# Performance work log

Measured on AMD Instinct MI355X. Metric: run time of the kernel, lower is better.

## Reference

```python
import math
import jax, jax.numpy as jnp
import numpy as np

# --- static config (matches init_kwargs) ---
BS, NIND, NSTEP, NDIM, ORDER, NEQ, NIVS, NIV = 128, 8, 64, 1, 2, 1, 2, 2
B = BS * NIND          # batch_size
K = ORDER + 1          # n_orders
S = NSTEP              # n_steps
T = S - 1
D = NDIM * K           # vars per step block
N = S * D              # total variables (without eps column)
NVARS = N + 1          # +1 eps column at index 0


def _smooth_indices():
    """Static (row, col) COO indices of the smoothness-constraint matrix,
    in the exact order the torch module emits values (forward, central, backward)."""
    def rav(st, dim, o):
        return (st * NDIM + dim) * K + o + 1  # +1 for eps column
    rows, cols, r = [], [], 0
    for st in range(T):                      # forward Taylor constraints
        for dim in range(NDIM):
            for i in range(K - 1):
                rows += [r, r]; cols += [0, rav(st + 1, dim, i)]
                for j in range(i, K):
                    rows.append(r); cols.append(rav(st, dim, j))
                r += 1
    for st in range(1, S - 1):               # central difference constraints
        for dim in range(NDIM):
            rows += [r] * 4
            cols += [0, rav(st - 1, dim, K - 2), rav(st + 1, dim, K - 2), rav(st, dim, K - 1)]
            r += 1
    for st in range(T):                      # backward Taylor constraints
        for dim in range(NDIM):
            for i in range(K - 1):
                rows += [r, r]; cols += [0, rav(st, dim, i)]
                for j in range(i, K):
                    rows.append(r); cols.append(rav(st + 1, dim, j))
                r += 1
    return np.asarray(rows), np.asarray(cols), r

ROWS, COLS, NROWS = _smooth_indices()
INIT_IDX = (np.arange(NDIM)[:, None] * K + np.arange(NIV)[None, :]).reshape(-1)
BLK = np.arange(S)[:, None] * D + np.arange(D)[None, :]  # (S, D) block row/col ids


def _derivative_A(steps):
    """Dense derivative-constraint matrix A: (B, NROWS, N) (eps column dropped)."""
    s = steps                                 # (B, T)
    ones = jnp.ones_like(s)
    fw, bw = [], []
    for i in range(K - 1):
        ss = -(s ** i)
        fw += [ones, ss]
        bw += [ones, ss if i % 2 == 0 else -ss]
        for j in range(i, K):
            v = s ** j / math.factorial(j - i)
            fw.append(v)
            bw.append(v if j % 2 == 0 else -v)
    fv = jnp.stack(fw, axis=-1).reshape(s.shape[0], -1)   # (B, T*L)
    bv = jnp.stack(bw, axis=-1).reshape(s.shape[0], -1)
    cp = s[:, 1:] + s[:, :-1]                             # csteps + psteps, (B, T-1)
    cv = jnp.stack([jnp.ones_like(cp), -cp ** (K - 3), cp ** (K - 3), -cp ** (K - 2)],
                   axis=-1).reshape(s.shape[0], -1)
    vals = jnp.concatenate([fv, cv, bv], axis=-1)          # (B, nnz)
    A_full = jnp.zeros((s.shape[0], NROWS, NVARS), dtype=s.dtype).at[:, ROWS, COLS].add(vals)
    return A_full[:, :, 1:]


def setup_inputs() -> dict:
    key = jax.random.key(0)
    k1, k2, k3, k4 = jax.random.split(key, 4)
    coeffs = jax.random.normal(k1, (B, S, NEQ, NDIM, K), dtype=jnp.float32)
    rhs = jax.random.normal(k2, (B, S, NEQ), dtype=jnp.float32)
    iv_rhs = jax.random.normal(k3, (B, NIVS, NDIM, NIV), dtype=jnp.float32)
    steps = jax.random.uniform(k4, (B, T), dtype=jnp.float32, minval=0.1, maxval=1.0)
    return {"coeffs": coeffs, "rhs": rhs, "iv_rhs": iv_rhs, "steps": steps}


def reference(coeffs, rhs, iv_rhs, steps):
    A = _derivative_A(steps)                                # (B, NROWS, N)
    Ae = coeffs.reshape(B, S, NEQ, D)
    AetAe = jnp.einsum('bsei,bsej->bsij', Ae, Ae)           # (B, S, D, D)
    Aetbe = jnp.einsum('bsei,bse->bsi', Ae, rhs)            # (B, S, D)
    # initial-value regularization on first NIVS step blocks
    AetAe = AetAe.at[:, :NIVS, INIT_IDX, INIT_IDX].add(1.0)
    bi = jnp.pad(iv_rhs, ((0, 0), (0, 0), (0, 0), (0, K - NIV))).reshape(B, NIVS, D)
    Aetbe = Aetbe.at[:, :NIVS, :].add(bi)
    # block-diagonal embedding of AetAe into the full NxN system
    dense = jnp.zeros((B, N, N), dtype=coeffs.dtype).at[:, BLK[:, :, None], BLK[:, None, :]].set(AetAe)
    AtA = jnp.einsum('bri,brj->bij', A, A) + dense          # (B, N, N) SPD
    Lc = jnp.linalg.cholesky(AtA)
    x = jax.scipy.linalg.cho_solve((Lc, True), Aetbe.reshape(B, N, 1))[..., 0]
    return x.reshape(B, S, NDIM, K)
```

## Files before the change

kernel.cpp:

```cpp
#include <hip/hip_runtime.h>
#include <math.h>

#define NB 1024
#define NS 64
#define NT 63
#define NV 192
#define BW 7
#define NC 314

#define NW 32
#define BP_PER_W (31*16)
#define L_PER_W  (93*8)
#define XQ_PER_W 96

__global__ __launch_bounds__(1024, 1)
void ode_mega(const float* __restrict__ coeffs,
              const float* __restrict__ rhs,
              const float* __restrict__ steps,
              const float* __restrict__ iv_rhs,
              float* __restrict__ wsBP,
              float* __restrict__ wsL,
              float* __restrict__ wsXq,
              float* __restrict__ out)
{
    const int w   = blockIdx.x;
    const int tid = threadIdx.x;

    __shared__ float cf[32 * 193];
    __shared__ float sl[32 * 65];
    __shared__ float rl[32 * 65];
    __shared__ float il[128];
    __shared__ float midl[27 * 32];
    __shared__ float mxl[6 * 32];

    for (int idx = tid; idx < 32 * 192; idx += 1024) {
        const int b = idx / 192, j = idx - 192 * b;
        cf[b * 193 + j] = coeffs[(size_t)w * 6144 + idx];
    }
    for (int idx = tid; idx < 32 * 63; idx += 1024) {
        const int b = idx / 63, j = idx - 63 * b;
        sl[b * 65 + j] = steps[(size_t)w * 2016 + idx];
    }
    for (int idx = tid; idx < 32 * 64; idx += 1024) {
        const int b = idx >> 6, j = idx & 63;
        rl[b * 65 + j] = rhs[(size_t)w * 2048 + idx];
    }
    if (tid < 128) il[tid] = iv_rhs[(size_t)w * 128 + tid];
    __syncthreads();

    for (int idx = tid; idx < 31 * 32; idx += 1024) {
        const int it = idx >> 5;
        const int pr = idx & 31;
        const float* cfp = cf + pr * 193;
        const float* slp = sl + pr * 65;
        const float* rlp = rl + pr * 65;

        float F[16], G[16];
        {
            const int t = it;
            const float c0 = cfp[3*t], c1 = cfp[3*t+1], c2 = cfp[3*t+2];
            const float r  = rlp[t];
            const float p  = (t >= 1) ? slp[t-1] : 0.f;
            const float s  = slp[t];
            const float sn = slp[t+1];
            const float mP = (t >= 1) ? 1.f : 0.f;
            const float rg = (t < 2) ? 1.f : 0.f;
            float iv0 = 0.f, iv1 = 0.f;
            if (t < 2) { iv0 = il[pr*4 + t*2]; iv1 = il[pr*4 + t*2 + 1]; }
            const float s2 = s*s, s3 = s2*s, p2 = p*p, p3 = p2*p, gt = p + s;
            F[0]  = c0*c0 + rg + 2.f*(1.f + mP);
            F[1]  = c0*c1 + s - p;
            F[2]  = c0*c2 + 0.5f*(s2 + p2);
            F[3]  = s;
            F[4]  = -0.5f*s2;
            F[5]  = c0*r + iv0;
            F[6]  = c1*c1 + 3.f*(s2 + p2) + 2.f;
            F[7]  = c1*c2 + 1.5f*(s3 - p3);
            F[8]  = -s;
            F[9]  = -2.f*s2;
            F[10] = s3 + (s + sn);
            F[11] = c1*r + iv1;
            F[12] = c2*c2 + 1.25f*(s2*s2 + p2*p2) + gt*gt*mP;
            F[13] = -0.5f*s2;
            F[14] = -s3 - gt*mP;
            F[15] = c2*r;
        }
        {
            const int t = 63 - it;
            const float c0 = cfp[3*t], c1 = cfp[3*t+1], c2 = cfp[3*t+2];
            const float r  = rlp[t];
            const float s  = (t < 63) ? slp[t] : 0.f;
            const float p  = slp[t-1];
            const float pp = slp[t-2];
            const float mSb  = (t < 63) ? 1.f : 0.f;
            const float mCNb = (t < 62) ? 1.f : 0.f;
            const float s2 = s*s, s3 = s2*s, p2 = p*p, p3 = p2*p, gt = p + s;
            G[0]  = c2*c2 + 1.25f*(s2*s2 + p2*p2) + gt*gt*mSb;
            G[1]  = c1*c2 + 1.5f*(s3 - p3);
            G[2]  = c0*c2 + 0.5f*(s2 + p2);
            G[3]  = p3 + (p + s)*mSb;
            G[4]  = -0.5f*p2;
            G[5]  = c2*r;
            G[6]  = c1*c1 + 3.f*(s2 + p2) + mCNb + 1.f;
            G[7]  = c0*c1 + s - p;
            G[8]  = -p3 - (pp + p);
            G[9]  = -2.f*p2;
            G[10] = p;
            G[11] = c1*r;
            G[12] = c0*c0 + 2.f*(mSb + 1.f);
            G[13] = -0.5f*p2;
            G[14] = -p;
            G[15] = c0*r;
        }
        float2* dst = (float2*)wsBP + ((size_t)w * BP_PER_W + (size_t)it * 16) * 32 + pr;
        #pragma unroll
        for (int k = 0; k < 16; ++k) dst[(size_t)k * 32] = make_float2(F[k], G[k]);
    }

    if (tid < 32) {
        const int pr = tid;
        const float* cfp = cf + pr * 193;
        const float* slp = sl + pr * 65;
        const float* rlp = rl + pr * 65;
        const float pA = slp[30], sA = slp[31], snA = slp[32];
        const float sB = slp[32], pB = sA;
        const float c0A = cfp[93], c1A = cfp[94], c2A = cfp[95];
        const float c0B = cfp[96], c1B = cfp[97], c2B = cfp[98];
        const float rA = rlp[31], rB = rlp[32];
        const float sA2 = sA*sA, sA3 = sA2*sA, pA2 = pA*pA, pA3 = pA2*pA;
        const float sB2 = sB*sB, sB3 = sB2*sB, pB2 = pB*pB, pB3 = pB2*pB;
        float m[27];
        m[0]  = c0A*c0A + 4.f;
        m[1]  = c0A*c1A + sA - pA;
        m[2]  = c0A*c2A + 0.5f*(sA2 + pA2);
        m[3]  = -2.f;
        m[4]  = sA;
        m[5]  = -0.5f*sA2;
        m[6]  = c1A*c1A + 3.f*(sA2 + pA2) + 2.f;
        m[7]  = c1A*c2A + 1.5f*(sA3 - pA3);
        m[8]  = -sA;
        m[9]  = -2.f*sA2;
        m[10] = sA3 + (sA + snA);
        m[11] = c2A*c2A + 1.25f*(sA2*sA2 + pA2*pA2) + (pA + sA)*(pA + sA);
        m[12] = -0.5f*sA2;
        m[13] = -sA3 - (pA + sA);
        m[14] = 0.f;
        m[15] = c0B*c0B + 4.f;
        m[16] = c0B*c1B + sB - pB;
        m[17] = c0B*c2B + 0.5f*(sB2 + pB2);
        m[18] = c1B*c1B + 3.f*(sB2 + pB2) + 2.f;
        m[19] = c1B*c2B + 1.5f*(sB3 - pB3);
        m[20] = c2B*c2B + 1.25f*(sB2*sB2 + pB2*pB2) + (pB + sB)*(pB + sB);
        m[21] = c0A*rA; m[22] = c1A*rA; m[23] = c2A*rA;
        m[24] = c0B*rB; m[25] = c1B*rB; m[26] = c2B*rB;
        #pragma unroll
        for (int k = 0; k < 27; ++k) midl[k * 32 + pr] = m[k];
    }

    __syncthreads();

    if (tid < 64) {
        const int l     = tid;
        const int pair  = l >> 1;
        const int chain = l & 1;
        const float cA  = chain ? 0.f : -2.f;
        const float cB  = chain ? -2.f : 0.f;

        const float* __restrict__ bp = wsBP + (size_t)w * BP_PER_W * 64 + l;
        float* __restrict__ ln = wsL  + (size_t)w * L_PER_W * 64 + l;
        float* __restrict__ xq = wsXq + (size_t)w * XQ_PER_W * 64 + l;

#define SBP(it, k) bp[(size_t)((it) * 16 + (k)) * 64]
#define SL(i)      ln[(size_t)(i) * 64]
#define SXQ(q)     xq[(size_t)(q) * 64]

        float W11=0,W12=0,W13=0,W14=0,W15=0,W16=0;
        float W22=0,W23=0,W24=0,W25=0,W26=0;
        float W33=0,W34=0,W35=0,W36=0;
        float W44=0,W45=0,W46=0;
        float W55=0,W56=0;
        float W66=0;
        float y1=0,y2=0,y3=0,y4=0,y5=0,y6=0;

#define CHOL_BODY(b0, b1, b2, b3, b4, b5, b6, rvv)                             \
        const float t0_ = (b0) - (W11*W11 + W22*W22 + W33*W33 +                \
                                  W44*W44 + W55*W55 + W66*W66);                \
        const float di_ = rsqrtf(t0_);                                         \
        const float u1_ = (b1) - (W11*W12 + W22*W23 + W33*W34 +                \
                                  W44*W45 + W55*W56);                          \
        const float u2_ = (b2) - (W11*W13 + W22*W24 + W33*W35 + W44*W46);      \
        const float u3_ = (b3) - (W11*W14 + W22*W25 + W33*W36);                \
        const float u4_ = (b4) - (W11*W15 + W22*W26);                          \
        const float u5_ = (b5) - (W11*W16);                                    \
        const float u6_ = (b6);                                                \
        const float yj_ = ((rvv) - (W11*y1 + W22*y2 + W33*y3 +                 \
                                    W44*y4 + W55*y5 + W66*y6)) * di_;          \
        const float n1_ = u1_*di_, n2_ = u2_*di_, n3_ = u3_*di_;               \
        const float n4_ = u4_*di_, n5_ = u5_*di_, n6_ = u6_*di_;

#define CHOL_SHIFT()                                                           \
        W66 = W56;                                                             \
        W55 = W45; W56 = W46;                                                  \
        W44 = W34; W45 = W35; W46 = W36;                                       \
        W33 = W23; W34 = W24; W35 = W25; W36 = W26;                            \
        W22 = W12; W23 = W13; W24 = W14; W25 = W15; W26 = W16;                 \
        W11 = n1_; W12 = n2_; W13 = n3_; W14 = n4_; W15 = n5_; W16 = n6_;      \
        y6 = y5; y5 = y4; y4 = y3; y3 = y2; y2 = y1; y1 = yj_;

#define CHOL_COL(q, b0, b1, b2, b3, b4, b5, b6, rvv)                           \
    {                                                                          \
        CHOL_BODY(b0, b1, b2, b3, b4, b5, b6, rvv)                             \
        SL((q)*8 + 0) = di_; SL((q)*8 + 1) = n1_; SL((q)*8 + 2) = n2_;         \
        SL((q)*8 + 3) = n3_; SL((q)*8 + 4) = n4_; SL((q)*8 + 5) = n5_;         \
        SL((q)*8 + 6) = n6_; SL((q)*8 + 7) = yj_;                              \
        CHOL_SHIFT()                                                           \
    }

#define CHOL_COL_CAP(P, b0, b1, b2, b3, b4, b5, b6, rvv)                       \
    {                                                                          \
        CHOL_BODY(b0, b1, b2, b3, b4, b5, b6, rvv)                             \
        P##d = di_; P##1 = n1_; P##2 = n2_; P##3 = n3_;                        \
        P##4 = n4_; P##5 = n5_; P##6 = n6_; P##y = yj_;                        \
        CHOL_SHIFT()                                                           \
    }

        float C0 = SBP(0,0),  C1 = SBP(0,1),  C2 = SBP(0,2),  C3 = SBP(0,3);
        float C4 = SBP(0,4),  C5 = SBP(0,5),  C6 = SBP(0,6),  C7 = SBP(0,7);
        float C8 = SBP(0,8),  C9 = SBP(0,9),  C10 = SBP(0,10), C11 = SBP(0,11);
        float C12 = SBP(0,12), C13 = SBP(0,13), C14 = SBP(0,14), C15 = SBP(0,15);
        float D0 = SBP(1,0),  D1 = SBP(1,1),  D2 = SBP(1,2),  D3 = SBP(1,3);
        float D4 = SBP(1,4),  D5 = SBP(1,5),  D6 = SBP(1,6),  D7 = SBP(1,7);
        float D8 = SBP(1,8),  D9 = SBP(1,9),  D10 = SBP(1,10), D11 = SBP(1,11);
        float D12 = SBP(1,12), D13 = SBP(1,13), D14 = SBP(1,14), D15 = SBP(1,15);

        for (int it = 0; it <= 29; ++it) {
            float N0=0,N1=0,N2=0,N3=0,N4=0,N5=0,N6=0,N7=0;
            float N8=0,N9=0,N10=0,N11=0,N12=0,N13=0,N14=0,N15=0;
            if (it + 2 <= 30) {
                N0  = SBP(it+2,0);  N1  = SBP(it+2,1);  N2  = SBP(it+2,2);  N3  = SBP(it+2,3);
                N4  = SBP(it+2,4);  N5  = SBP(it+2,5);  N6  = SBP(it+2,6);  N7  = SBP(it+2,7);
                N8  = SBP(it+2,8);  N9  = SBP(it+2,9);  N10 = SBP(it+2,10); N11 = SBP(it+2,11);
                N12 = SBP(it+2,12); N13 = SBP(it+2,13); N14 = SBP(it+2,14); N15 = SBP(it+2,15);
            }
            const int q0 = 3 * it;
            CHOL_COL(q0 + 0, C0,  C1,  C2,  cA,   C3,  C4,  0.f,  C5);
            CHOL_COL(q0 + 1, C6,  C7,  C8,  C9,   C10, 0.f, -1.f, C11);
            CHOL_COL(q0 + 2, C12, C13, C14, cB,   0.f, 0.f, 0.f,  C15);
            C0=D0; C1=D1; C2=D2; C3=D3; C4=D4; C5=D5; C6=D6; C7=D7;
            C8=D8; C9=D9; C10=D10; C11=D11; C12=D12; C13=D13; C14=D14; C15=D15;
            D0=N0; D1=N1; D2=N2; D3=N3; D4=N4; D5=N5; D6=N6; D7=N7;
            D8=N8; D9=N9; D10=N10; D11=N11; D12=N12; D13=N13; D14=N14; D15=N15;
        }

#define DECL8(P) float P##d = 0, P##1 = 0, P##2 = 0, P##3 = 0,                 \
                       P##4 = 0, P##5 = 0, P##6 = 0, P##y = 0;
#define LOAD8(P, q) { const size_t o8 = (size_t)(q)*8;                         \
        P##d = SL(o8 + 0); P##1 = SL(o8 + 1); P##2 = SL(o8 + 2);               \
        P##3 = SL(o8 + 3); P##4 = SL(o8 + 4); P##5 = SL(o8 + 5);               \
        P##6 = SL(o8 + 6); P##y = SL(o8 + 7); }

        DECL8(PA) DECL8(PB) DECL8(PC)
        DECL8(QA) DECL8(QB) DECL8(QC)
        DECL8(RA) DECL8(RB) DECL8(RC)

        CHOL_COL_CAP(PA, C0,  C1,  C2,  cA,   C3,  C4,  0.f,  C5);
        CHOL_COL_CAP(PB, C6,  C7,  C8,  C9,   C10, 0.f, -1.f, C11);
        CHOL_COL_CAP(PC, C12, C13, C14, cB,   0.f, 0.f, 0.f,  C15);

        LOAD8(QC, 89) LOAD8(QB, 88) LOAD8(QA, 87)
        LOAD8(RC, 86) LOAD8(RB, 85) LOAD8(RA, 84)

        const float R11=__shfl_xor(W11,1), R12=__shfl_xor(W12,1), R13=__shfl_xor(W13,1);
        const float R14=__shfl_xor(W14,1), R15=__shfl_xor(W15,1), R16=__shfl_xor(W16,1);
        const float R22=__shfl_xor(W22,1), R23=__shfl_xor(W23,1), R24=__shfl_xor(W24,1);
        const float R25=__shfl_xor(W25,1), R26=__shfl_xor(W26,1);
        const float R33=__shfl_xor(W33,1), R34=__shfl_xor(W34,1), R35=__shfl_xor(W35,1);
        const float R36=__shfl_xor(W36,1);
        const float R44=__shfl_xor(W44,1), R45=__shfl_xor(W45,1), R46=__shfl_xor(W46,1);
        const float R55=__shfl_xor(W55,1), R56=__shfl_xor(W56,1);
        const float R66=__shfl_xor(W66,1);
        const float r1=__shfl_xor(y1,1), r2=__shfl_xor(y2,1), r3=__shfl_xor(y3,1);
        const float r4=__shfl_xor(y4,1), r5=__shfl_xor(y5,1), r6=__shfl_xor(y6,1);

        float xm0=0, xm1=0, xm2=0, xm3=0, xm4=0, xm5=0;
        if (chain == 0) {
            const float* __restrict__ md = midl + pair;
            float S00 = md[0*32],  S10 = md[1*32],  S20 = md[2*32];
            float S30 = md[3*32],  S40 = md[4*32],  S50 = md[5*32];
            float S11 = md[6*32],  S21 = md[7*32],  S31 = md[8*32];
            float S41 = md[9*32],  S51 = md[10*32], S22 = md[11*32];
            float S32 = md[12*32], S42 = md[13*32], S52 = md[14*32];
            float S33 = md[15*32], S43 = md[16*32], S53 = md[17*32];
            float S44 = md[18*32], S54 = md[19*32], S55 = md[20*32];
            float fm0 = md[21*32], fm1 = md[22*32], fm2 = md[23*32];
            float fm3 = md[24*32], fm4 = md[25*32], fm5 = md[26*32];

            S00 -= W11*W11 + W22*W22 + W33*W33 + W44*W44 + W55*W55 + W66*W66;
            S10 -= W12*W11 + W23*W22 + W34*W33 + W45*W44 + W56*W55;
            S11 -= W12*W12 + W23*W23 + W34*W34 + W45*W45 + W56*W56;
            S20 -= W13*W11 + W24*W22 + W35*W33 + W46*W44;
            S21 -= W13*W12 + W24*W23 + W35*W34 + W46*W45;
            S22 -= W13*W13 + W24*W24 + W35*W35 + W46*W46;
            S30 -= W14*W11 + W25*W22 + W36*W33;
            S31 -= W14*W12 + W25*W23 + W36*W34;
            S32 -= W14*W13 + W25*W24 + W36*W35;
            S33 -= W14*W14 + W25*W25 + W36*W36;
            S40 -= W15*W11 + W26*W22;
            S41 -= W15*W12 + W26*W23;
            S42 -= W15*W13 + W26*W24;
            S43 -= W15*W14 + W26*W25;
            S44 -= W15*W15 + W26*W26;
            S50 -= W16*W11;
            S51 -= W16*W12;
            S52 -= W16*W13;
            S53 -= W16*W14;
            S54 -= W16*W15;
            S55 -= W16*W16;

            S00 -= R16*R16;
            S10 -= R15*R16;
            S11 -= R15*R15 + R26*R26;
            S20 -= R14*R16;
            S21 -= R14*R15 + R25*R26;
            S22 -= R14*R14 + R25*R25 + R36*R36;
            S30 -= R13*R16;
            S31 -= R13*R15 + R24*R26;
            S32 -= R13*R14 + R24*R25 + R35*R36;
            S33 -= R13*R13 + R24*R24 + R35*R35 + R46*R46;
            S40 -= R12*R16;
            S41 -= R12*R15 + R23*R26;
            S42 -= R12*R14 + R23*R25 + R34*R36;
            S43 -= R12*R13 + R23*R24 + R34*R35 + R45*R46;
            S44 -= R12*R12 + R23*R23 + R34*R34 + R45*R45 + R56*R56;
            S50 -= R11*R16;
            S51 -= R11*R15 + R22*R26;
            S52 -= R11*R14 + R22*R25 + R33*R36;
            S53 -= R11*R13 + R22*R24 + R33*R35 + R44*R46;
            S54 -= R11*R12 + R22*R23 + R33*R34 + R44*R45 + R55*R56;
            S55 -= R11*R11 + R22*R22 + R33*R33 + R44*R44 + R55*R55 + R66*R66;

            fm0 -= (W11*y1 + W22*y2 + W33*y3 + W44*y4 + W55*y5 + W66*y6) + (R16*r1);
            fm1 -= (W12*y1 + W23*y2 + W34*y3 + W45*y4 + W56*y5) + (R15*r1 + R26*r2);
            fm2 -= (W13*y1 + W24*y2 + W35*y3 + W46*y4) + (R14*r1 + R25*r2 + R36*r3);
            fm3 -= (W14*y1 + W25*y2 + W36*y3) + (R13*r1 + R24*r2 + R35*r3 + R46*r4);
            fm4 -= (W15*y1 + W26*y2) + (R12*r1 + R23*r2 + R34*r3 + R45*r4 + R56*r5);
            fm5 -= (W16*y1) + (R11*r1 + R22*r2 + R33*r3 + R44*r4 + R55*r5 + R66*r6);

            const float md0 = rsqrtf(S00);
            const float M10 = S10*md0, M20 = S20*md0, M30 = S30*md0,
                        M40 = S40*md0, M50 = S50*md0;
            const float zm0 = fm0*md0;
            const float md1 = rsqrtf(S11 - M10*M10);
            const float M21 = (S21 - M20*M10)*md1;
            const float M31 = (S31 - M30*M10)*md1;
            const float M41 = (S41 - M40*M10)*md1;
            const float M51 = (S51 - M50*M10)*md1;
            const float zm1 = (fm1 - M10*zm0)*md1;
            const float md2 = rsqrtf(S22 - M20*M20 - M21*M21);
            const float M32 = (S32 - M30*M20 - M31*M21)*md2;
            const float M42 = (S42 - M40*M20 - M41*M21)*md2;
            const float M52 = (S52 - M50*M20 - M51*M21)*md2;
            const float zm2 = (fm2 - M20*zm0 - M21*zm1)*md2;
            const float md3 = rsqrtf(S33 - M30*M30 - M31*M31 - M32*M32);
            const float M43 = (S43 - M40*M30 - M41*M31 - M42*M32)*md3;
            const float M53 = (S53 - M50*M30 - M51*M31 - M52*M32)*md3;
            const float zm3 = (fm3 - M30*zm0 - M31*zm1 - M32*zm2)*md3;
            const float md4 = rsqrtf(S44 - M40*M40 - M41*M41 - M42*M42 - M43*M43);
            const float M54 = (S54 - M50*M40 - M51*M41 - M52*M42 - M53*M43)*md4;
            const float zm4 = (fm4 - M40*zm0 - M41*zm1 - M42*zm2 - M43*zm3)*md4;
            const float md5 = rsqrtf(S55 - M50*M50 - M51*M51 - M52*M52 - M53*M53 - M54*M54);
            const float zm5 = (fm5 - M50*zm0 - M51*zm1 - M52*zm2 - M53*zm3 - M54*zm4)*md5;

            xm5 = zm5*md5;
            xm4 = (zm4 - M54*xm5)*md4;
            xm3 = (zm3 - M43*xm4 - M53*xm5)*md3;
            xm2 = (zm2 - M32*xm3 - M42*xm4 - M52*xm5)*md2;
            xm1 = (zm1 - M21*xm2 - M31*xm3 - M41*xm4 - M51*xm5)*md1;
            xm0 = (zm0 - M10*xm1 - M20*xm2 - M30*xm3 - M40*xm4 - M50*xm5)*md0;

            mxl[0*32 + pair] = xm0; mxl[1*32 + pair] = xm1; mxl[2*32 + pair] = xm2;
            mxl[3*32 + pair] = xm3; mxl[4*32 + pair] = xm4; mxl[5*32 + pair] = xm5;
        }

        const float g0 = __shfl_xor(xm0, 1), g1 = __shfl_xor(xm1, 1);
        const float g2 = __shfl_xor(xm2, 1), g3 = __shfl_xor(xm3, 1);
        const float g4 = __shfl_xor(xm4, 1), g5 = __shfl_xor(xm5, 1);

        float x1 = chain ? g5 : xm0;
        float x2 = chain ? g4 : xm1;
        float x3 = chain ? g3 : xm2;
        float x4 = chain ? g2 : xm3;
        float x5 = chain ? g1 : xm4;
        float x6 = chain ? g0 : xm5;

#define BSUB(P, q) {                                                           \
        const float rest = (P##6*x6 + P##5*x5) + (P##4*x4 + P##3*x3) + P##2*x2;\
        const float xr = ((P##y - rest) - P##1*x1) * P##d;                     \
        SXQ(q) = xr;                                                           \
        x6 = x5; x5 = x4; x4 = x3; x3 = x2; x2 = x1; x1 = xr; }

        for (int it2 = 0; it2 < 31; it2 += 3) {
            {   const int st = 30 - it2;
                BSUB(PC, 3*st + 2) BSUB(PB, 3*st + 1) BSUB(PA, 3*st)
                if (st - 3 >= 0) { LOAD8(PC, 3*(st-3) + 2) LOAD8(PB, 3*(st-3) + 1) LOAD8(PA, 3*(st-3)) }
            }
            {   const int st = 29 - it2;
                if (st >= 0) {
                    BSUB(QC, 3*st + 2) BSUB(QB, 3*st + 1) BSUB(QA, 3*st)
                    if (st - 3 >= 0) { LOAD8(QC, 3*(st-3) + 2) LOAD8(QB, 3*(st-3) + 1) LOAD8(QA, 3*(st-3)) }
                }
            }
            {   const int st = 28 - it2;
                if (st >= 0) {
                    BSUB(RC, 3*st + 2) BSUB(RB, 3*st + 1) BSUB(RA, 3*st)
                    if (st - 3 >= 0) { LOAD8(RC, 3*(st-3) + 2) LOAD8(RB, 3*(st-3) + 1) LOAD8(RA, 3*(st-3)) }
                }
            }
        }

#undef SBP
#undef SL
#undef SXQ
#undef CHOL_BODY
#undef CHOL_SHIFT
#undef CHOL_COL
#undef CHOL_COL_CAP
#undef DECL8
#undef LOAD8
#undef BSUB
    }

    __syncthreads();

    {
        const float* __restrict__ xg = wsXq + (size_t)w * XQ_PER_W * 64;
        for (int idx = tid; idx < 32 * 192; idx += 1024) {
            const int bl = idx / 192;
            const int j  = idx - bl * 192;
            float v;
            if (j < 93)      v = xg[(size_t)j * 64 + 2 * bl];
            else if (j > 98) v = xg[(size_t)(191 - j) * 64 + 2 * bl + 1];
            else             v = mxl[(j - 93) * 32 + bl];
            out[(size_t)w * 6144 + idx] = v;
        }
    }
}

__global__ __launch_bounds__(64, 1)
void ode_banded_solve(const float* __restrict__ coeffs,
                      const float* __restrict__ rhs,
                      const float* __restrict__ iv_rhs,
                      const float* __restrict__ steps,
                      float* __restrict__ out)
{
    const int b    = blockIdx.x;
    const int lane = threadIdx.x;

    __shared__ float band[NV * BW];
    __shared__ float rv[NV];
    __shared__ float stp[NT + 1];

    for (int i = lane; i < NV * BW; i += 64) band[i] = 0.0f;
    if (lane < NT) stp[lane] = steps[b * NT + lane];
    __syncthreads();

    {
        const int st = lane;
        const float c0 = coeffs[b * NV + st * 3 + 0];
        const float c1 = coeffs[b * NV + st * 3 + 1];
        const float c2 = coeffs[b * NV + st * 3 + 2];
        const float r  = rhs[b * NS + st];
        const float reg = (st < 2) ? 1.0f : 0.0f;
        atomicAdd(&band[(3 * st + 0) * BW + 0], c0 * c0 + reg);
        atomicAdd(&band[(3 * st + 1) * BW + 0], c1 * c1 + reg);
        atomicAdd(&band[(3 * st + 2) * BW + 0], c2 * c2);
        atomicAdd(&band[(3 * st + 1) * BW + 1], c1 * c0);
        atomicAdd(&band[(3 * st + 2) * BW + 1], c2 * c1);
        atomicAdd(&band[(3 * st + 2) * BW + 2], c2 * c0);
        float b0 = c0 * r, b1 = c1 * r, b2v = c2 * r;
        if (st < 2) {
            b0 += iv_rhs[b * 4 + st * 2 + 0];
            b1 += iv_rhs[b * 4 + st * 2 + 1];
        }
        rv[3 * st + 0] = b0;
        rv[3 * st + 1] = b1;
        rv[3 * st + 2] = b2v;
    }

    for (int t = lane; t < NC; t += 64) {
        int   cols[4];
        float vals[4];
        int   cnt;
        if (t < 126) {
            const int st = t >> 1, i = t & 1;
            const float s = stp[st];
            if (i == 0) {
                cols[0] = 3 * st + 0; vals[0] = 1.0f;
                cols[1] = 3 * st + 1; vals[1] = s;
                cols[2] = 3 * st + 2; vals[2] = 0.5f * s * s;
                cols[3] = 3 * st + 3; vals[3] = -1.0f;
                cnt = 4;
            } else {
                cols[0] = 3 * st + 1; vals[0] = s;
                cols[1] = 3 * st + 2; vals[1] = s * s;
                cols[2] = 3 * st + 4; vals[2] = -s;
                cnt = 3;
            }
        } else if (t < 188) {
            const int st = t - 126 + 1;
            const float cp = stp[st - 1] + stp[st];
            cols[0] = 3 * st - 2; vals[0] = -1.0f;
            cols[1] = 3 * st + 2; vals[1] = -cp;
            cols[2] = 3 * st + 4; vals[2] = 1.0f;
            cnt = 3;
        } else {
            const int tt = t - 188;
            const int st = tt >> 1, i = tt & 1;
            const float s = stp[st];
            if (i == 0) {
                cols[0] = 3 * st + 0; vals[0] = -1.0f;
                cols[1] = 3 * st + 3; vals[1] = 1.0f;
                cols[2] = 3 * st + 4; vals[2] = -s;
                cols[3] = 3 * st + 5; vals[3] = 0.5f * s * s;
                cnt = 4;
            } else {
                cols[0] = 3 * st + 1; vals[0] = s;
                cols[1] = 3 * st + 4; vals[1] = -s;
                cols[2] = 3 * st + 5; vals[2] = s * s;
                cnt = 3;
            }
        }
        for (int a = 0; a < cnt; ++a)
            for (int b2 = 0; b2 <= a; ++b2)
                atomicAdd(&band[cols[a] * BW + (cols[a] - cols[b2])],
                          vals[a] * vals[b2]);
    }
    __syncthreads();

    int pa = 0, pb = 0;
    {
        int idx = 0;
        for (int aa = 1; aa <= 6; ++aa)
            for (int bb = 1; bb <= aa; ++bb) {
                if (idx == lane) { pa = aa; pb = bb; }
                ++idx;
            }
    }
    const int sk = lane - 20;

    for (int j = 0; j < NV; ++j) {
        const int m = (NV - 1 - j < 6) ? (NV - 1 - j) : 6;
        const float diag = band[j * BW];
        const float d    = sqrtf(diag);
        const float dinv = 1.0f / d;

        const bool doU = (lane < 21) && (pa <= m);
        const bool doS = (lane >= 21) && (lane <= 26) && (sk <= m);
        float ca = 0.0f, cb = 0.0f, cs = 0.0f;
        if (doU) { ca = band[(j + pa) * BW + pa]; cb = band[(j + pb) * BW + pb]; }
        if (doS) { cs = band[(j + sk) * BW + sk]; }
        __syncthreads();

        if (lane == 0) band[j * BW] = d;
        if (doU) band[(j + pa) * BW + (pa - pb)] -= ca * cb * (dinv * dinv);
        if (doS) band[(j + sk) * BW + sk] = cs * dinv;
        __syncthreads();
    }

    for (int j = 0; j < NV; ++j) {
        const int m = (NV - 1 - j < 6) ? (NV - 1 - j) : 6;
        const float yj = rv[j] / band[j * BW];
        const bool doK = (lane >= 1) && (lane <= m);
        float sub = 0.0f, rj = 0.0f;
        if (doK) { sub = band[(j + lane) * BW + lane] * yj; rj = rv[j + lane]; }
        __syncthreads();
        if (lane == 0) rv[j] = yj;
        if (doK) rv[j + lane] = rj - sub;
        __syncthreads();
    }

    for (int j = NV - 1; j >= 0; --j) {
        const int m = (j < 6) ? j : 6;
        const float xj = rv[j] / band[j * BW];
        const bool doK = (lane >= 1) && (lane <= m);
        float sub = 0.0f, rj = 0.0f;
        if (doK) { sub = band[j * BW + lane] * xj; rj = rv[j - lane]; }
        __syncthreads();
        if (lane == 0) rv[j] = xj;
        if (doK) rv[j - lane] = rj - sub;
        __syncthreads();
    }

    for (int i = lane; i < NV; i += 64)
        out[b * NV + i] = rv[i];
}

extern "C" void kernel_launch(void* const* d_in, const int* in_sizes, int n_in,
                              void* d_out, int out_size, void* d_ws, size_t ws_size,
                              hipStream_t stream)
{
    const float* coeffs = (const float*)d_in[0];
    const float* rhs    = (const float*)d_in[1];
    const float* iv_rhs = (const float*)d_in[2];
    const float* steps  = (const float*)d_in[3];
    float* out = (float*)d_out;

    const size_t BPf = (size_t)NW * BP_PER_W * 64;
    const size_t Lf  = (size_t)NW * L_PER_W * 64;
    const size_t XQf = (size_t)NW * XQ_PER_W * 64;
    const size_t need = (BPf + Lf + XQf) * sizeof(float);

    if (ws_size >= need) {
        float* wsBP = (float*)d_ws;
        float* wsL  = wsBP + BPf;
        float* wsXq = wsL  + Lf;
        ode_mega<<<dim3(NW), dim3(1024), 0, stream>>>(coeffs, rhs, steps, iv_rhs,
                                                      wsBP, wsL, wsXq, out);
    } else {
        ode_banded_solve<<<dim3(NB), dim3(64), 0, stream>>>(coeffs, rhs, iv_rhs,
                                                            steps, out);
    }
}
```

Before: 44.30 us.

## Halve problems per block, double grid, keep Cholesky factors in LDS

The kernel now uses 64 blocks of 256 threads, each handling 16 problems, instead of 32 blocks of 1024 threads handling 32. Each block's 32-lane solver warp stores its Cholesky factor and forward-substitution vector in shared memory rather than in global workspace. This spreads the sequential solve over more CUs and replaces global round-trips on the latency-critical chain with LDS accesses. The cost is larger LDS per block (about 100KB) and fewer threads per block for the parallel setup phase.

```diff
diff --git a/kernel.cpp b/kernel.cpp
--- a/kernel.cpp
+++ b/kernel.cpp
@@ -8,49 +8,48 @@
 #define BW 7
 #define NC 314
 
-#define NW 32
-#define BP_PER_W (31*16)
-#define L_PER_W  (93*8)
-#define XQ_PER_W 96
-
-__global__ __launch_bounds__(1024, 1)
-void ode_mega(const float* __restrict__ coeffs,
-              const float* __restrict__ rhs,
-              const float* __restrict__ steps,
-              const float* __restrict__ iv_rhs,
-              float* __restrict__ wsBP,
-              float* __restrict__ wsL,
-              float* __restrict__ wsXq,
-              float* __restrict__ out)
+#define NBLK 64
+#define PB 16
+#define BP_SLOTS (31*16)
+
+__global__ __launch_bounds__(256, 1)
+void ode_mega2(const float* __restrict__ coeffs,
+               const float* __restrict__ rhs,
+               const float* __restrict__ steps,
+               const float* __restrict__ iv_rhs,
+               float* __restrict__ wsBP,
+               float* __restrict__ out)
 {
     const int w   = blockIdx.x;
     const int tid = threadIdx.x;
 
-    __shared__ float cf[32 * 193];
-    __shared__ float sl[32 * 65];
-    __shared__ float rl[32 * 65];
-    __shared__ float il[128];
-    __shared__ float midl[27 * 32];
-    __shared__ float mxl[6 * 32];
-
-    for (int idx = tid; idx < 32 * 192; idx += 1024) {
+    __shared__ float cf[PB * 193];
+    __shared__ float sl[PB * 65];
+    __shared__ float rl[PB * 65];
+    __shared__ float il[PB * 4];
+    __shared__ float midl[27 * PB];
+    __shared__ float mxl[6 * PB];
+    __shared__ float lql[93 * 8 * 32];
+    __shared__ float xql[93 * 32];
+
+    for (int idx = tid; idx < PB * 192; idx += 256) {
         const int b = idx / 192, j = idx - 192 * b;
-        cf[b * 193 + j] = coeffs[(size_t)w * 6144 + idx];
-    }
-    for (int idx = tid; idx < 32 * 63; idx += 1024) {
+        cf[b * 193 + j] = coeffs[(size_t)w * (PB * 192) + idx];
+    }
+    for (int idx = tid; idx < PB * 63; idx += 256) {
         const int b = idx / 63, j = idx - 63 * b;
-        sl[b * 65 + j] = steps[(size_t)w * 2016 + idx];
-    }
-    for (int idx = tid; idx < 32 * 64; idx += 1024) {
+        sl[b * 65 + j] = steps[(size_t)w * (PB * 63) + idx];
+    }
+    for (int idx = tid; idx < PB * 64; idx += 256) {
         const int b = idx >> 6, j = idx & 63;
-        rl[b * 65 + j] = rhs[(size_t)w * 2048 + idx];
-    }
-    if (tid < 128) il[tid] = iv_rhs[(size_t)w * 128 + tid];
+        rl[b * 65 + j] = rhs[(size_t)w * (PB * 64) + idx];
+    }
+    if (tid < PB * 4) il[tid] = iv_rhs[(size_t)w * (PB * 4) + tid];
     __syncthreads();
 
-    for (int idx = tid; idx < 31 * 32; idx += 1024) {
-        const int it = idx >> 5;
-        const int pr = idx & 31;
+    for (int idx = tid; idx < 31 * PB; idx += 256) {
+        const int it = idx >> 4;
+        const int pr = idx & 15;
         const float* cfp = cf + pr * 193;
         const float* slp = sl + pr * 65;
         const float* rlp = rl + pr * 65;
@@ -112,23 +111,24 @@
             G[14] = -p;
             G[15] = c0*r;
         }
-        float2* dst = (float2*)wsBP + ((size_t)w * BP_PER_W + (size_t)it * 16) * 32 + pr;
+        float2* dst = (float2*)wsBP + (size_t)w * (BP_SLOTS * 16)
+                                    + (size_t)it * 256 + pr;
         #pragma unroll
-        for (int k = 0; k < 16; ++k) dst[(size_t)k * 32] = make_float2(F[k], G[k]);
-    }
-
-    if (tid < 32) {
+        for (int k = 0; k < 16; ++k) dst[(size_t)k * 16] = make_float2(F[k], G[k]);
+    }
+
+    if (tid < PB) {
         const int pr = tid;
         const float* cfp = cf + pr * 193;
         const float* slp = sl + pr * 65;
         const float* rlp = rl + pr * 65;
         const float pA = slp[30], sA = slp[31], snA = slp[32];
-        const float sB = slp[32], pB = sA;
+        const float sB = slp[32], pB2_ = sA;
         const float c0A = cfp[93], c1A = cfp[94], c2A = cfp[95];
         const float c0B = cfp[96], c1B = cfp[97], c2B = cfp[98];
         const float rA = rlp[31], rB = rlp[32];
         const float sA2 = sA*sA, sA3 = sA2*sA, pA2 = pA*pA, pA3 = pA2*pA;
-        const float sB2 = sB*sB, sB3 = sB2*sB, pB2 = pB*pB, pB3 = pB2*pB;
+        const float sB2 = sB*sB, sB3 = sB2*sB, pB2 = pB2_*pB2_, pB3 = pB2*pB2_;
         float m[27];
         m[0]  = c0A*c0A + 4.f;
         m[1]  = c0A*c1A + sA - pA;
@@ -146,33 +146,31 @@
         m[13] = -sA3 - (pA + sA);
         m[14] = 0.f;
         m[15] = c0B*c0B + 4.f;
-        m[16] = c0B*c1B + sB - pB;
+        m[16] = c0B*c1B + sB - pB2_;
         m[17] = c0B*c2B + 0.5f*(sB2 + pB2);
         m[18] = c1B*c1B + 3.f*(sB2 + pB2) + 2.f;
         m[19] = c1B*c2B + 1.5f*(sB3 - pB3);
-        m[20] = c2B*c2B + 1.25f*(sB2*sB2 + pB2*pB2) + (pB + sB)*(pB + sB);
+        m[20] = c2B*c2B + 1.25f*(sB2*sB2 + pB2*pB2) + (pB2_ + sB)*(pB2_ + sB);
         m[21] = c0A*rA; m[22] = c1A*rA; m[23] = c2A*rA;
         m[24] = c0B*rB; m[25] = c1B*rB; m[26] = c2B*rB;
         #pragma unroll
-        for (int k = 0; k < 27; ++k) midl[k * 32 + pr] = m[k];
+        for (int k = 0; k < 27; ++k) midl[k * PB + pr] = m[k];
     }
 
     __syncthreads();
 
-    if (tid < 64) {
+    if (tid < 32) {
         const int l     = tid;
         const int pair  = l >> 1;
         const int chain = l & 1;
         const float cA  = chain ? 0.f : -2.f;
         const float cB  = chain ? -2.f : 0.f;
 
-        const float* __restrict__ bp = wsBP + (size_t)w * BP_PER_W * 64 + l;
-        float* __restrict__ ln = wsL  + (size_t)w * L_PER_W * 64 + l;
-        float* __restrict__ xq = wsXq + (size_t)w * XQ_PER_W * 64 + l;
-
-#define SBP(it, k) bp[(size_t)((it) * 16 + (k)) * 64]
-#define SL(i)      ln[(size_t)(i) * 64]
-#define SXQ(q)     xq[(size_t)(q) * 64]
+        const float* __restrict__ bp = wsBP + (size_t)w * (BP_SLOTS * 32) + l;
+
+#define SBP(it, k) bp[(size_t)(((it) * 16 + (k)) * 32)]
+#define SL(i)      lql[(i) * 32 + l]
+#define SXQ(q)     xql[(q) * 32 + l]
 
         float W11=0,W12=0,W13=0,W14=0,W15=0,W16=0;
         float W22=0,W23=0,W24=0,W25=0,W26=0;
@@ -254,18 +252,18 @@
 
 #define DECL8(P) float P##d = 0, P##1 = 0, P##2 = 0, P##3 = 0,                 \
                        P##4 = 0, P##5 = 0, P##6 = 0, P##y = 0;
-#define LOAD8(P, q) { const size_t o8 = (size_t)(q)*8;                         \
+#define LOAD8(P, q) { const int o8 = (q)*8;                                    \
         P##d = SL(o8 + 0); P##1 = SL(o8 + 1); P##2 = SL(o8 + 2);               \
         P##3 = SL(o8 + 3); P##4 = SL(o8 + 4); P##5 = SL(o8 + 5);               \
         P##6 = SL(o8 + 6); P##y = SL(o8 + 7); }
 
-        DECL8(PA) DECL8(PB) DECL8(PC)
+        DECL8(PA) DECL8(PB_) DECL8(PC)
         DECL8(QA) DECL8(QB) DECL8(QC)
         DECL8(RA) DECL8(RB) DECL8(RC)
 
-        CHOL_COL_CAP(PA, C0,  C1,  C2,  cA,   C3,  C4,  0.f,  C5);
-        CHOL_COL_CAP(PB, C6,  C7,  C8,  C9,   C10, 0.f, -1.f, C11);
-        CHOL_COL_CAP(PC, C12, C13, C14, cB,   0.f, 0.f, 0.f,  C15);
+        CHOL_COL_CAP(PA,  C0,  C1,  C2,  cA,   C3,  C4,  0.f,  C5);
+        CHOL_COL_CAP(PB_, C6,  C7,  C8,  C9,   C10, 0.f, -1.f, C11);
+        CHOL_COL_CAP(PC,  C12, C13, C14, cB,   0.f, 0.f, 0.f,  C15);
 
         LOAD8(QC, 89) LOAD8(QB, 88) LOAD8(QA, 87)
         LOAD8(RC, 86) LOAD8(RB, 85) LOAD8(RA, 84)
@@ -285,15 +283,15 @@
         float xm0=0, xm1=0, xm2=0, xm3=0, xm4=0, xm5=0;
         if (chain == 0) {
             const float* __restrict__ md = midl + pair;
-            float S00 = md[0*32],  S10 = md[1*32],  S20 = md[2*32];
-            float S30 = md[3*32],  S40 = md[4*32],  S50 = md[5*32];
-            float S11 = md[6*32],  S21 = md[7*32],  S31 = md[8*32];
-            float S41 = md[9*32],  S51 = md[10*32], S22 = md[11*32];
-            float S32 = md[12*32], S42 = md[13*32], S52 = md[14*32];
-            float S33 = md[15*32], S43 = md[16*32], S53 = md[17*32];
-            float S44 = md[18*32], S54 = md[19*32], S55 = md[20*32];
-            float fm0 = md[21*32], fm1 = md[22*32], fm2 = md[23*32];
-            float fm3 = md[24*32], fm4 = md[25*32], fm5 = md[26*32];
+            float S00 = md[0*PB],  S10 = md[1*PB],  S20 = md[2*PB];
+            float S30 = md[3*PB],  S40 = md[4*PB],  S50 = md[5*PB];
+            float S11 = md[6*PB],  S21 = md[7*PB],  S31 = md[8*PB];
+            float S41 = md[9*PB],  S51 = md[10*PB], S22 = md[11*PB];
+            float S32 = md[12*PB], S42 = md[13*PB], S52 = md[14*PB];
+            float S33 = md[15*PB], S43 = md[16*PB], S53 = md[17*PB];
+            float S44 = md[18*PB], S54 = md[19*PB], S55 = md[20*PB];
+            float fm0 = md[21*PB], fm1 = md[22*PB], fm2 = md[23*PB];
+            float fm3 = md[24*PB], fm4 = md[25*PB], fm5 = md[26*PB];
 
             S00 -= W11*W11 + W22*W22 + W33*W33 + W44*W44 + W55*W55 + W66*W66;
             S10 -= W12*W11 + W23*W22 + W34*W33 + W45*W44 + W56*W55;
@@ -378,8 +376,8 @@
             xm1 = (zm1 - M21*xm2 - M31*xm3 - M41*xm4 - M51*xm5)*md1;
             xm0 = (zm0 - M10*xm1 - M20*xm2 - M30*xm3 - M40*xm4 - M50*xm5)*md0;
 
-            mxl[0*32 + pair] = xm0; mxl[1*32 + pair] = xm1; mxl[2*32 + pair] = xm2;
-            mxl[3*32 + pair] = xm3; mxl[4*32 + pair] = xm4; mxl[5*32 + pair] = xm5;
+            mxl[0*PB + pair] = xm0; mxl[1*PB + pair] = xm1; mxl[2*PB + pair] = xm2;
+            mxl[3*PB + pair] = xm3; mxl[4*PB + pair] = xm4; mxl[5*PB + pair] = xm5;
         }
 
         const float g0 = __shfl_xor(xm0, 1), g1 = __shfl_xor(xm1, 1);
@@ -401,8 +399,8 @@
 
         for (int it2 = 0; it2 < 31; it2 += 3) {
             {   const int st = 30 - it2;
-                BSUB(PC, 3*st + 2) BSUB(PB, 3*st + 1) BSUB(PA, 3*st)
-                if (st - 3 >= 0) { LOAD8(PC, 3*(st-3) + 2) LOAD8(PB, 3*(st-3) + 1) LOAD8(PA, 3*(st-3)) }
+                BSUB(PC, 3*st + 2) BSUB(PB_, 3*st + 1) BSUB(PA, 3*st)
+                if (st - 3 >= 0) { LOAD8(PC, 3*(st-3) + 2) LOAD8(PB_, 3*(st-3) + 1) LOAD8(PA, 3*(st-3)) }
             }
             {   const int st = 29 - it2;
                 if (st >= 0) {
@@ -432,17 +430,14 @@
 
     __syncthreads();
 
-    {
-        const float* __restrict__ xg = wsXq + (size_t)w * XQ_PER_W * 64;
-        for (int idx = tid; idx < 32 * 192; idx += 1024) {
-            const int bl = idx / 192;
-            const int j  = idx - bl * 192;
-            float v;
-            if (j < 93)      v = xg[(size_t)j * 64 + 2 * bl];
-            else if (j > 98) v = xg[(size_t)(191 - j) * 64 + 2 * bl + 1];
-            else             v = mxl[(j - 93) * 32 + bl];
-            out[(size_t)w * 6144 + idx] = v;
-        }
+    for (int idx = tid; idx < PB * 192; idx += 256) {
+        const int bl = idx / 192;
+        const int j  = idx - bl * 192;
+        float v;
+        if (j < 93)      v = xql[j * 32 + 2 * bl];
+        else if (j > 98) v = xql[(191 - j) * 32 + 2 * bl + 1];
+        else             v = mxl[(j - 93) * PB + bl];
+        out[(size_t)w * (PB * 192) + idx] = v;
     }
 }
 
@@ -605,17 +600,11 @@
     const float* steps  = (const float*)d_in[3];
     float* out = (float*)d_out;
 
-    const size_t BPf = (size_t)NW * BP_PER_W * 64;
-    const size_t Lf  = (size_t)NW * L_PER_W * 64;
-    const size_t XQf = (size_t)NW * XQ_PER_W * 64;
-    const size_t need = (BPf + Lf + XQf) * sizeof(float);
+    const size_t need = (size_t)NBLK * BP_SLOTS * 32 * sizeof(float);
 
     if (ws_size >= need) {
-        float* wsBP = (float*)d_ws;
-        float* wsL  = wsBP + BPf;
-        float* wsXq = wsL  + Lf;
-        ode_mega<<<dim3(NW), dim3(1024), 0, stream>>>(coeffs, rhs, steps, iv_rhs,
-                                                      wsBP, wsL, wsXq, out);
+        ode_mega2<<<dim3(NBLK), dim3(256), 0, stream>>>(coeffs, rhs, steps, iv_rhs,
+                                                        (float*)d_ws, out);
     } else {
         ode_banded_solve<<<dim3(NB), dim3(64), 0, stream>>>(coeffs, rhs, iv_rhs,
                                                             steps, out);
```

New measurement: 41.08 us. -7.3%, faster.
